# Kernel optimization log

Measured on AMD Instinct MI355X. Metric: run time of the kernel, lower is better.

## Reference

```python
import jax, jax.numpy as jnp
import numpy as np

D_MODEL = 1024
N_HEADS = 16
DEPTH = D_MODEL // N_HEADS
DFF = 4096
B, S = 2, 2048
EPS = 1e-6


def layer_norm(x, gamma, beta):
    m = jnp.mean(x, axis=-1, keepdims=True)
    v = jnp.mean(jnp.square(x - m), axis=-1, keepdims=True)
    return (x - m) * jax.lax.rsqrt(v + EPS) * gamma + beta


def setup_inputs() -> dict:
    key = jax.random.key(0)
    ks = jax.random.split(key, 16)
    s = 0.02
    x = jax.random.normal(ks[0], (B, S, D_MODEL), dtype=jnp.float32)
    # causal mask: 1.0 where attention is NOT allowed (upper triangle)
    mask = (1.0 - jnp.tril(jnp.ones((S, S), dtype=jnp.float32)))[None, None, :, :]
    return {
        "x": x,
        "mask": mask,
        "wq": jax.random.normal(ks[1], (D_MODEL, D_MODEL), jnp.float32) * s,
        "bq": jnp.zeros((D_MODEL,), jnp.float32),
        "wk": jax.random.normal(ks[2], (D_MODEL, D_MODEL), jnp.float32) * s,
        "bk": jnp.zeros((D_MODEL,), jnp.float32),
        "wv": jax.random.normal(ks[3], (D_MODEL, D_MODEL), jnp.float32) * s,
        "bv": jnp.zeros((D_MODEL,), jnp.float32),
        "wo": jax.random.normal(ks[4], (D_MODEL, D_MODEL), jnp.float32) * s,
        "bo": jnp.zeros((D_MODEL,), jnp.float32),
        "g1": jnp.ones((D_MODEL,), jnp.float32),
        "be1": jnp.zeros((D_MODEL,), jnp.float32),
        "w1": jax.random.normal(ks[5], (D_MODEL, DFF), jnp.float32) * s,
        "b1": jnp.zeros((DFF,), jnp.float32),
        "w2": jax.random.normal(ks[6], (DFF, D_MODEL), jnp.float32) * s,
        "b2": jnp.zeros((D_MODEL,), jnp.float32),
        "g2": jnp.ones((D_MODEL,), jnp.float32),
        "be2": jnp.zeros((D_MODEL,), jnp.float32),
    }


def reference(x, mask, wq, bq, wk, bk, wv, bv, wo, bo, g1, be1, w1, b1, w2, b2, g2, be2):
    b, s = x.shape[0], x.shape[1]

    def heads(t):  # [B,S,D_MODEL] -> [B,H,S,depth]
        return t.reshape(b, s, N_HEADS, DEPTH).transpose(0, 2, 1, 3)

    q = heads(x @ wq + bq)
    k = heads(x @ wk + bk)
    v = heads(x @ wv + bv)

    # [B,H,S,S] scores, materialized as in the original
    logits = jnp.einsum("bhqd,bhkd->bhqk", q, k) / jnp.sqrt(jnp.float32(DEPTH))
    logits = logits + mask * (-1e9)
    attn = jax.nn.softmax(logits, axis=-1)
    ctx = jnp.einsum("bhqk,bhkd->bhqd", attn, v)
    ctx = ctx.transpose(0, 2, 1, 3).reshape(b, s, D_MODEL)
    attn_out = ctx @ wo + bo

    out1 = layer_norm(x + attn_out, g1, be1)
    ffn = jax.nn.relu(out1 @ w1 + b1) @ w2 + b2
    out2 = layer_norm(out1 + ffn, g2, be2)
    return out2  # dropout inactive (training=False)
```

## Files before the change

### kernel.cpp

```cpp
#include <hip/hip_runtime.h>
#include <stdint.h>

typedef unsigned short u16;
typedef unsigned int u32;
typedef __attribute__((ext_vector_type(8))) short short8;
typedef __attribute__((ext_vector_type(4))) float f32x4;

#define NHEADS 16
#define SEQ 2048
#define DM 1024
#define MROWS 4096
#define FF 4096

static_assert(sizeof(short8) == 16, "short8 must be 16B");

__device__ __forceinline__ u16 f2b(float f) {
  u32 u = __float_as_uint(f);
  u += 0x7fffu + ((u >> 16) & 1u);
  return (u16)(u >> 16);
}
__device__ __forceinline__ u32 f2b2(float lo, float hi) {
  u32 a = __float_as_uint(lo); a += 0x7fffu + ((a >> 16) & 1u);
  u32 b = __float_as_uint(hi); b += 0x7fffu + ((b >> 16) & 1u);
  return (a >> 16) | (b & 0xffff0000u);
}
__device__ __forceinline__ float b2f(u16 h) { return __uint_as_float(((u32)h) << 16); }

__device__ __forceinline__ void async_cp16(const u16* g, u16* l) {
  __builtin_amdgcn_global_load_lds((const __attribute__((address_space(1))) void*)g,
                                   (__attribute__((address_space(3))) void*)l, 16, 0, 0);
}

__global__ __launch_bounds__(256) void prep_k(const float* __restrict__ x,
                                              const float* __restrict__ wq,
                                              const float* __restrict__ wk,
                                              const float* __restrict__ wv,
                                              const float* __restrict__ wo,
                                              const float* __restrict__ w1,
                                              const float* __restrict__ w2,
                                              u16* __restrict__ xb, u16* __restrict__ btq,
                                              u16* __restrict__ wot, u16* __restrict__ w1t,
                                              u16* __restrict__ w2t) {
  const int bid = blockIdx.x, tid = threadIdx.x;
  if (bid < 4096) {
    const int i = bid * 256 + tid;
    const float4 v = ((const float4*)x)[i];
    uint2 o; o.x = f2b2(v.x, v.y); o.y = f2b2(v.z, v.w);
    ((uint2*)xb)[i] = o;
    return;
  }
  __shared__ float tile[32][33];
  const int tb = bid - 4096;
  const float* in; u16* out; int N, K, n0, k0;
  if (tb < 4096) {
    const int m = tb >> 10, t = tb & 1023;
    if (m == 0) { in = wq; out = btq; }
    else if (m == 1) { in = wk; out = btq + 1024 * 1024; }
    else if (m == 2) { in = wv; out = btq + 2 * 1024 * 1024; }
    else { in = wo; out = wot; }
    N = 1024; K = 1024; n0 = (t & 31) * 32; k0 = (t >> 5) * 32;
  } else if (tb < 8192) {
    const int t = tb - 4096;
    in = w1; out = w1t; N = 4096; K = 1024; n0 = (t & 127) * 32; k0 = (t >> 7) * 32;
  } else {
    const int t = tb - 8192;
    in = w2; out = w2t; N = 1024; K = 4096; n0 = (t & 31) * 32; k0 = (t >> 5) * 32;
  }
  const int tx = tid & 31, ty = tid >> 5;
#pragma unroll
  for (int i = 0; i < 4; i++) {
    const int r = ty + i * 8;
    tile[r][tx] = in[(long)(k0 + r) * N + n0 + tx];
  }
  __syncthreads();
#pragma unroll
  for (int i = 0; i < 4; i++) {
    const int r = ty + i * 8;
    out[(long)(n0 + r) * K + k0 + tx] = f2b(tile[tx][r]);
  }
}

template <typename TIN>
__global__ __launch_bounds__(256) void transpose_bf16(const TIN* __restrict__ in,
                                                      u16* __restrict__ out, const int K,
                                                      const int N, const long isz, const long osz) {
  __shared__ float tile[32][33];
  const TIN* inz = in + (long)blockIdx.z * isz;
  u16* outz = out + (long)blockIdx.z * osz;
  const int n0 = blockIdx.x * 32, k0 = blockIdx.y * 32;
  const int tx = threadIdx.x & 31, ty = threadIdx.x >> 5;
#pragma unroll
  for (int i = 0; i < 4; i++) {
    const int r = ty + i * 8;
    float val;
    if constexpr (sizeof(TIN) == 4) { val = inz[(long)(k0 + r) * N + n0 + tx]; }
    else { val = b2f(inz[(long)(k0 + r) * N + n0 + tx]); }
    tile[r][tx] = val;
  }
  __syncthreads();
#pragma unroll
  for (int i = 0; i < 4; i++) {
    const int r = ty + i * 8;
    outz[(long)(n0 + r) * K + k0 + tx] = f2b(tile[tx][r]);
  }
}

#define BM 128
#define BN 128
#define BK 64
#define EPI_QKV 0
#define EPI_RELUB 2
#define EPI_PART 3

template <int EPI>
__global__ __launch_bounds__(256, 2) void gemm_bt(
    const u16* __restrict__ A, const u16* __restrict__ Bt, const int M, const int N,
    const int KITER, const int LDA, const int KOFF,
    const float* __restrict__ bias0, const float* __restrict__ bias1,
    const float* __restrict__ bias2,
    float* __restrict__ outF, u16* __restrict__ outB, u16* __restrict__ outQ,
    u16* __restrict__ outK, u16* __restrict__ outV) {
  __shared__ u16 As[BM * BK];
  __shared__ u16 Bs[BN * BK];
  const int tid = threadIdx.x;
  const int lane = tid & 63;
  const int wv = tid >> 6;
  const int quad = lane >> 4;
  const int lm = lane & 15;
  const int tn = blockIdx.x * BN;
  const int tm = blockIdx.y * BM;
  const int wr = (wv >> 1) * 64;
  const int wc = (wv & 1) * 64;
  const int wslotbase = tid & ~63;
  const long zoff = (long)blockIdx.z * KOFF;
  const u16* Ap = A + zoff;
  const u16* Btp = Bt + zoff;

  const f32x4 z4 = {0.f, 0.f, 0.f, 0.f};
  f32x4 acc[4][4];
#pragma unroll
  for (int i = 0; i < 4; i++)
#pragma unroll
    for (int j = 0; j < 4; j++) acc[i][j] = z4;

  for (int kk = 0; kk < KITER; kk += BK) {
    __syncthreads();
#pragma unroll
    for (int t = 0; t < 4; t++) {
      const int slot = t * 256 + tid;
      const int row = slot >> 3;
      const int c = (slot & 7) ^ (row & 7);
      async_cp16(Ap + (long)(tm + row) * LDA + kk + c * 8,
                 As + (long)(t * 256 + wslotbase) * 8);
    }
#pragma unroll
    for (int t = 0; t < 4; t++) {
      const int slot = t * 256 + tid;
      const int row = slot >> 3;
      const int c = (slot & 7) ^ (row & 7);
      async_cp16(Btp + (long)(tn + row) * LDA + kk + c * 8,
                 Bs + (long)(t * 256 + wslotbase) * 8);
    }
    __syncthreads();
#pragma unroll
    for (int ks = 0; ks < 2; ks++) {
      short8 af[4], bf[4];
#pragma unroll
      for (int mi = 0; mi < 4; mi++) {
        const int row = wr + mi * 16 + lm;
        const int cc = (4 * ks + quad) ^ (row & 7);
        af[mi] = *(const short8*)(As + row * 64 + cc * 8);
      }
#pragma unroll
      for (int ni = 0; ni < 4; ni++) {
        const int row = wc + ni * 16 + lm;
        const int cc = (4 * ks + quad) ^ (row & 7);
        bf[ni] = *(const short8*)(Bs + row * 64 + cc * 8);
      }
#pragma unroll
      for (int mi = 0; mi < 4; mi++)
#pragma unroll
        for (int ni = 0; ni < 4; ni++)
          acc[mi][ni] =
              __builtin_amdgcn_mfma_f32_16x16x32_bf16(af[mi], bf[ni], acc[mi][ni], 0, 0, 0);
    }
  }

  if constexpr (EPI == EPI_QKV) {
    const int which = tn >> 10;
    const float* bs = which == 0 ? bias0 : (which == 1 ? bias1 : bias2);
    u16* os = which == 0 ? outQ : (which == 1 ? outK : outV);
    const float scale = which == 0 ? 0.125f * 1.44269504f : 1.0f;
#pragma unroll
    for (int ni = 0; ni < 4; ni++) {
      const int n = tn + wc + ni * 16 + lm;
      const int hd = n & 1023;
      const int h = hd >> 6, dep = hd & 63;
      const float bval = bs[hd];
#pragma unroll
      for (int mi = 0; mi < 4; mi++) {
#pragma unroll
        for (int r = 0; r < 4; r++) {
          const int m = tm + wr + mi * 16 + quad * 4 + r;
          const int bb = m >> 11, ss = m & 2047;
          os[(((long)(bb * NHEADS + h) * SEQ + ss) << 6) + dep] =
              f2b((acc[mi][ni][r] + bval) * scale);
        }
      }
    }
  } else if constexpr (EPI == EPI_PART) {
    float* po = outF + (long)blockIdx.z * M * N;
#pragma unroll
    for (int mi = 0; mi < 4; mi++) {
#pragma unroll
      for (int r = 0; r < 4; r++) {
        const int m = tm + wr + mi * 16 + quad * 4 + r;
        const long rowo = (long)m * N;
#pragma unroll
        for (int ni = 0; ni < 4; ni++) {
          const int n = tn + wc + ni * 16 + lm;
          po[rowo + n] = acc[mi][ni][r];
        }
      }
    }
  } else {
#pragma unroll
    for (int mi = 0; mi < 4; mi++) {
#pragma unroll
      for (int r = 0; r < 4; r++) {
        const int m = tm + wr + mi * 16 + quad * 4 + r;
        const long rowo = (long)m * N;
#pragma unroll
        for (int ni = 0; ni < 4; ni++) {
          const int n = tn + wc + ni * 16 + lm;
          const float v = acc[mi][ni][r] + bias0[n];
          outB[rowo + n] = f2b(fmaxf(v, 0.f));
        }
      }
    }
  }
}

__global__ __launch_bounds__(256, 3) void attn_fused(const u16* __restrict__ Q,
                                                     const u16* __restrict__ K,
                                                     const u16* __restrict__ Vt,
                                                     u16* __restrict__ O,
                                                     float* __restrict__ part,
                                                     float* __restrict__ lpart) {
  __shared__ u16 Ks[2][64 * 64];
  __shared__ u16 Vs[2][64 * 64];
  __shared__ u16 Ps[4][16 * 72];
  const int tid = threadIdx.x;
  const int lane = tid & 63, w = tid >> 6, quad = lane >> 4, lm = lane & 15;
  const int bid = blockIdx.x;
  const int idx = bid >> 5, hb = bid & 31;
  const int h = hb & 15, b = hb >> 4;
  int qt, c0, nkl, half;
  if (idx < 32) {
    qt = 16 + (idx >> 1);
    const int nk = qt + 1;
    const int h0 = (nk + 1) >> 1;
    half = idx & 1;
    if (half == 0) { c0 = 0; nkl = h0; } else { c0 = h0; nkl = nk - h0; }
  } else {
    qt = 47 - idx; c0 = 0; nkl = qt + 1; half = -1;
  }
  const long bh = (long)(b * NHEADS + h);
  const u16* Qb = Q + bh * SEQ * 64;
  const u16* Kb = K + bh * SEQ * 64;
  const u16* Vb = Vt + bh * (long)64 * SEQ;
  const int rbase = qt * 64 + w * 16;
  const int wslot = tid & ~63;

  short8 qf[2];
#pragma unroll
  for (int ks = 0; ks < 2; ks++)
    qf[ks] = *(const short8*)(Qb + (long)(rbase + lm) * 64 + ks * 32 + quad * 8);

  const f32x4 z4 = {0.f, 0.f, 0.f, 0.f};
  f32x4 ctx[4];
#pragma unroll
  for (int d = 0; d < 4; d++) ctx[d] = z4;
  float lacc = 0.f;
  u16* myP = (u16*)Ps[w];

  {
    const int k0p = c0 * 64;
#pragma unroll
    for (int i = 0; i < 2; i++) {
      const int slot = i * 256 + tid;
      const int row = slot >> 3;
      const int cg = (slot & 7) ^ (row & 7);
      async_cp16(Kb + (long)(k0p + row) * 64 + cg * 8, Ks[0] + (i * 256 + wslot) * 8);
      async_cp16(Vb + (long)row * SEQ + k0p + cg * 8, Vs[0] + (i * 256 + wslot) * 8);
    }
  }

  for (int t = 0; t < nkl; t++) {
    const int cur = t & 1;
    const int k0 = (c0 + t) * 64;
    __syncthreads();
    if (t + 1 < nkl) {
      const int kn = k0 + 64;
#pragma unroll
      for (int i = 0; i < 2; i++) {
        const int slot = i * 256 + tid;
        const int row = slot >> 3;
        const int cg = (slot & 7) ^ (row & 7);
        async_cp16(Kb + (long)(kn + row) * 64 + cg * 8, Ks[1 - cur] + (i * 256 + wslot) * 8);
        async_cp16(Vb + (long)row * SEQ + kn + cg * 8, Vs[1 - cur] + (i * 256 + wslot) * 8);
      }
    }
    const u16* Kc = Ks[cur];
    const u16* Vc = Vs[cur];
    short8 kf[4][2];
#pragma unroll
    for (int ni = 0; ni < 4; ni++) {
      const int row = ni * 16 + lm;
      const int r8 = row & 7;
#pragma unroll
      for (int ks = 0; ks < 2; ks++) {
        const int cc = (ks * 4 + quad) ^ r8;
        kf[ni][ks] = *(const short8*)(Kc + row * 64 + cc * 8);
      }
    }
    f32x4 sa[4];
#pragma unroll
    for (int i = 0; i < 4; i++) sa[i] = z4;
#pragma unroll
    for (int ks = 0; ks < 2; ks++)
#pragma unroll
      for (int ni = 0; ni < 4; ni++)
        sa[ni] = __builtin_amdgcn_mfma_f32_16x16x32_bf16(kf[ni][ks], qf[ks], sa[ni], 0, 0, 0);
    const int qrow = rbase + lm;
    if (k0 + 63 > rbase) {
#pragma unroll
      for (int ni = 0; ni < 4; ni++)
#pragma unroll
        for (int r = 0; r < 4; r++)
          if (k0 + ni * 16 + quad * 4 + r > qrow) sa[ni][r] = -1e9f;
    }
    float tsum = 0.f;
#pragma unroll
    for (int ni = 0; ni < 4; ni++) {
      const float p0 = exp2f(sa[ni][0]);
      const float p1 = exp2f(sa[ni][1]);
      const float p2 = exp2f(sa[ni][2]);
      const float p3 = exp2f(sa[ni][3]);
      tsum += (p0 + p1) + (p2 + p3);
      uint2 o; o.x = f2b2(p0, p1); o.y = f2b2(p2, p3);
      *(uint2*)(myP + lm * 72 + ni * 16 + quad * 4) = o;
    }
    lacc += tsum;
#pragma unroll
    for (int kc = 0; kc < 2; kc++) {
      const short8 bp = *(const short8*)(myP + lm * 72 + kc * 32 + quad * 8);
#pragma unroll
      for (int dni = 0; dni < 4; dni++) {
        const int row = dni * 16 + lm;
        const int cc = (kc * 4 + quad) ^ (row & 7);
        const short8 vfr = *(const short8*)(Vc + row * 64 + cc * 8);
        ctx[dni] = __builtin_amdgcn_mfma_f32_16x16x32_bf16(vfr, bp, ctx[dni], 0, 0, 0);
      }
    }
  }
  float l = lacc;
  l += __shfl_xor(l, 16);
  l += __shfl_xor(l, 32);
  if (half < 0) {
    const float inv = 1.0f / l;
    const int s = rbase + lm;
    const long base = (long)(b * SEQ + s) * DM + h * 64;
#pragma unroll
    for (int dni = 0; dni < 4; dni++) {
      uint2 o;
      o.x = f2b2(ctx[dni][0] * inv, ctx[dni][1] * inv);
      o.y = f2b2(ctx[dni][2] * inv, ctx[dni][3] * inv);
      *(uint2*)(O + base + dni * 16 + quad * 4) = o;
    }
  } else {
    const long pt = ((long)(hb * 16 + (qt - 16))) * 2 + half;
    float* po = part + pt * 4096 + (w * 16 + lm) * 64;
#pragma unroll
    for (int dni = 0; dni < 4; dni++)
      *(float4*)(po + dni * 16 + quad * 4) =
          make_float4(ctx[dni][0], ctx[dni][1], ctx[dni][2], ctx[dni][3]);
    if (quad == 0) lpart[pt * 64 + w * 16 + lm] = l;
  }
}

__global__ __launch_bounds__(256) void attn_combine(const float* __restrict__ part,
                                                    const float* __restrict__ lpart,
                                                    u16* __restrict__ O) {
  const int g = blockIdx.x;
  const int hb = g >> 4, qtr = g & 15;
  const int h = hb & 15, b = hb >> 4;
  const int qt = 16 + qtr;
  const long pt0 = ((long)(hb * 16 + qtr)) * 2;
  const float* p0 = part + pt0 * 4096;
  const float* p1 = p0 + 4096;
  const float* lp = lpart + pt0 * 64;
  const int tid = threadIdx.x;
  const int row = tid >> 2, d0 = (tid & 3) * 16;
  const float inv = 1.0f / (lp[row] + lp[64 + row]);
  const long off = (long)(b * SEQ + qt * 64 + row) * DM + h * 64 + d0;
  u32 o[8];
#pragma unroll
  for (int i = 0; i < 4; i++) {
    const float4 a = *(const float4*)(p0 + row * 64 + d0 + i * 4);
    const float4 c = *(const float4*)(p1 + row * 64 + d0 + i * 4);
    o[i * 2 + 0] = f2b2((a.x + c.x) * inv, (a.y + c.y) * inv);
    o[i * 2 + 1] = f2b2((a.z + c.z) * inv, (a.w + c.w) * inv);
  }
  *(uint4*)(O + off) = make_uint4(o[0], o[1], o[2], o[3]);
  *(uint4*)(O + off + 8) = make_uint4(o[4], o[5], o[6], o[7]);
}

template <bool WB>
__global__ __launch_bounds__(256) void layernorm2_k(const float* __restrict__ p0,
                                                    const float* __restrict__ p1,
                                                    const float* __restrict__ resid,
                                                    const float* __restrict__ bias,
                                                    const float* __restrict__ gam,
                                                    const float* __restrict__ bet,
                                                    float* __restrict__ outF,
                                                    u16* __restrict__ outB) {
  __shared__ float red[8];
  const int row = blockIdx.x, tid = threadIdx.x;
  const long off = (long)row * DM;
  const float4 a4 = ((const float4*)(p0 + off))[tid];
  const float4 b4v = ((const float4*)(p1 + off))[tid];
  const float4 r4 = ((const float4*)(resid + off))[tid];
  const float4 bi4 = ((const float4*)bias)[tid];
  float4 v;
  v.x = a4.x + b4v.x + r4.x + bi4.x;
  v.y = a4.y + b4v.y + r4.y + bi4.y;
  v.z = a4.z + b4v.z + r4.z + bi4.z;
  v.w = a4.w + b4v.w + r4.w + bi4.w;
  float s1 = v.x + v.y + v.z + v.w;
  float s2 = v.x * v.x + v.y * v.y + v.z * v.z + v.w * v.w;
  s1 += __shfl_xor(s1, 1); s2 += __shfl_xor(s2, 1);
  s1 += __shfl_xor(s1, 2); s2 += __shfl_xor(s2, 2);
  s1 += __shfl_xor(s1, 4); s2 += __shfl_xor(s2, 4);
  s1 += __shfl_xor(s1, 8); s2 += __shfl_xor(s2, 8);
  s1 += __shfl_xor(s1, 16); s2 += __shfl_xor(s2, 16);
  s1 += __shfl_xor(s1, 32); s2 += __shfl_xor(s2, 32);
  if ((tid & 63) == 0) { red[tid >> 6] = s1; red[4 + (tid >> 6)] = s2; }
  __syncthreads();
  const float mean = (red[0] + red[1] + red[2] + red[3]) * (1.f / DM);
  const float ex2 = (red[4] + red[5] + red[6] + red[7]) * (1.f / DM);
  const float var = fmaxf(ex2 - mean * mean, 0.f);
  const float rs = rsqrtf(var + 1e-6f);
  const float4 g4 = ((const float4*)gam)[tid];
  const float4 be4 = ((const float4*)bet)[tid];
  const float o0 = (v.x - mean) * rs * g4.x + be4.x;
  const float o1 = (v.y - mean) * rs * g4.y + be4.y;
  const float o2 = (v.z - mean) * rs * g4.z + be4.z;
  const float o3 = (v.w - mean) * rs * g4.w + be4.w;
  ((float4*)(outF + off))[tid] = make_float4(o0, o1, o2, o3);
  if constexpr (WB) {
    uint2 o; o.x = f2b2(o0, o1); o.y = f2b2(o2, o3);
    ((uint2*)(outB + off))[tid] = o;
  }
}

extern "C" void kernel_launch(void* const* d_in, const int* in_sizes, int n_in,
                              void* d_out, int out_size, void* d_ws, size_t ws_size,
                              hipStream_t stream) {
  (void)in_sizes; (void)n_in; (void)out_size; (void)ws_size;
  const float* x = (const float*)d_in[0];
  const float* wq = (const float*)d_in[2];
  const float* bq = (const float*)d_in[3];
  const float* wk = (const float*)d_in[4];
  const float* bk = (const float*)d_in[5];
  const float* wv = (const float*)d_in[6];
  const float* bv = (const float*)d_in[7];
  const float* wo = (const float*)d_in[8];
  const float* bo = (const float*)d_in[9];
  const float* g1 = (const float*)d_in[10];
  const float* be1 = (const float*)d_in[11];
  const float* w1 = (const float*)d_in[12];
  const float* b1 = (const float*)d_in[13];
  const float* w2 = (const float*)d_in[14];
  const float* b2 = (const float*)d_in[15];
  const float* g2 = (const float*)d_in[16];
  const float* be2 = (const float*)d_in[17];
  float* out = (float*)d_out;
  uint8_t* ws = (uint8_t*)d_ws;
  const size_t MB = 1024ull * 1024ull;
  u16* wot = (u16*)(ws + 0 * MB);
  u16* w1t = (u16*)(ws + 2 * MB);
  u16* w2t = (u16*)(ws + 10 * MB);
  u16* btq = (u16*)(ws + 18 * MB);
  u16* xb  = (u16*)(ws + 24 * MB);
  u16* qb  = (u16*)(ws + 32 * MB);
  u16* kb  = (u16*)(ws + 40 * MB);
  u16* vb  = (u16*)(ws + 48 * MB);
  u16* vt  = (u16*)(ws + 56 * MB);
  u16* ctxb = (u16*)(ws + 64 * MB);
  float* part = (float*)(ws + 72 * MB);
  float* apart = (float*)(ws + 72 * MB);
  float* lpart = (float*)(ws + 89 * MB);
  u16* o1b = (u16*)(ws + 104 * MB);
  float* o1f = (float*)(ws + 112 * MB);
  u16* h1 = (u16*)(ws + 18 * MB);

  prep_k<<<dim3(16384), dim3(256), 0, stream>>>(x, wq, wk, wv, wo, w1, w2, xb, btq, wot,
                                                w1t, w2t);

  gemm_bt<EPI_QKV><<<dim3(24, 32), dim3(256), 0, stream>>>(
      xb, btq, MROWS, 3072, 1024, 1024, 0, bq, bk, bv, nullptr, nullptr, qb, kb, vb);

  transpose_bf16<u16><<<dim3(2, 64, 32), dim3(256), 0, stream>>>(
      vb, vt, 2048, 64, (long)2048 * 64, (long)64 * 2048);

  attn_fused<<<dim3(1536), dim3(256), 0, stream>>>(qb, kb, vt, ctxb, apart, lpart);
  attn_combine<<<dim3(512), dim3(256), 0, stream>>>(apart, lpart, ctxb);

  gemm_bt<EPI_PART><<<dim3(8, 32, 2), dim3(256), 0, stream>>>(
      ctxb, wot, MROWS, 1024, 512, 1024, 512, nullptr, nullptr, nullptr, part, nullptr,
      nullptr, nullptr, nullptr);

  layernorm2_k<true><<<dim3(4096), dim3(256), 0, stream>>>(
      part, part + (long)MROWS * DM, x, bo, g1, be1, o1f, o1b);

  gemm_bt<EPI_RELUB><<<dim3(32, 32), dim3(256), 0, stream>>>(
      o1b, w1t, MROWS, 4096, 1024, 1024, 0, b1, nullptr, nullptr, nullptr, h1, nullptr,
      nullptr, nullptr);

  gemm_bt<EPI_PART><<<dim3(8, 32, 2), dim3(256), 0, stream>>>(
      h1, w2t, MROWS, 1024, 2048, 4096, 2048, nullptr, nullptr, nullptr, part, nullptr,
      nullptr, nullptr, nullptr);

  layernorm2_k<false><<<dim3(4096), dim3(256), 0, stream>>>(
      part, part + (long)MROWS * DM, o1f, b2, g2, be2, out, nullptr);
}
```

Before: 357.7 us.

## Fuse V transpose into QKV epilogue, drop split-K partials, add residual in GEMM

```diff
diff --git a/kernel.cpp b/kernel.cpp
--- a/kernel.cpp
+++ b/kernel.cpp
@@ -23,6 +23,9 @@
   u32 a = __float_as_uint(lo); a += 0x7fffu + ((a >> 16) & 1u);
   u32 b = __float_as_uint(hi); b += 0x7fffu + ((b >> 16) & 1u);
   return (a >> 16) | (b & 0xffff0000u);
+}
+__device__ __forceinline__ u32 f2b2t(float lo, float hi) {
+  return __builtin_amdgcn_perm(__float_as_uint(hi), __float_as_uint(lo), 0x07060302u);
 }
 __device__ __forceinline__ float b2f(u16 h) { return __uint_as_float(((u32)h) << 16); }
 
@@ -80,44 +83,18 @@
   }
 }
 
-template <typename TIN>
-__global__ __launch_bounds__(256) void transpose_bf16(const TIN* __restrict__ in,
-                                                      u16* __restrict__ out, const int K,
-                                                      const int N, const long isz, const long osz) {
-  __shared__ float tile[32][33];
-  const TIN* inz = in + (long)blockIdx.z * isz;
-  u16* outz = out + (long)blockIdx.z * osz;
-  const int n0 = blockIdx.x * 32, k0 = blockIdx.y * 32;
-  const int tx = threadIdx.x & 31, ty = threadIdx.x >> 5;
-#pragma unroll
-  for (int i = 0; i < 4; i++) {
-    const int r = ty + i * 8;
-    float val;
-    if constexpr (sizeof(TIN) == 4) { val = inz[(long)(k0 + r) * N + n0 + tx]; }
-    else { val = b2f(inz[(long)(k0 + r) * N + n0 + tx]); }
-    tile[r][tx] = val;
-  }
-  __syncthreads();
-#pragma unroll
-  for (int i = 0; i < 4; i++) {
-    const int r = ty + i * 8;
-    outz[(long)(n0 + r) * K + k0 + tx] = f2b(tile[tx][r]);
-  }
-}
-
 #define BM 128
 #define BN 128
 #define BK 64
 #define EPI_QKV 0
+#define EPI_ADDRES 1
 #define EPI_RELUB 2
-#define EPI_PART 3
 
 template <int EPI>
 __global__ __launch_bounds__(256, 2) void gemm_bt(
     const u16* __restrict__ A, const u16* __restrict__ Bt, const int M, const int N,
-    const int KITER, const int LDA, const int KOFF,
-    const float* __restrict__ bias0, const float* __restrict__ bias1,
-    const float* __restrict__ bias2,
+    const int K, const float* __restrict__ bias0, const float* __restrict__ bias1,
+    const float* __restrict__ bias2, const float* __restrict__ resid,
     float* __restrict__ outF, u16* __restrict__ outB, u16* __restrict__ outQ,
     u16* __restrict__ outK, u16* __restrict__ outV) {
   __shared__ u16 As[BM * BK];
@@ -132,9 +109,6 @@
   const int wr = (wv >> 1) * 64;
   const int wc = (wv & 1) * 64;
   const int wslotbase = tid & ~63;
-  const long zoff = (long)blockIdx.z * KOFF;
-  const u16* Ap = A + zoff;
-  const u16* Btp = Bt + zoff;
 
   const f32x4 z4 = {0.f, 0.f, 0.f, 0.f};
   f32x4 acc[4][4];
@@ -143,14 +117,14 @@
 #pragma unroll
     for (int j = 0; j < 4; j++) acc[i][j] = z4;
 
-  for (int kk = 0; kk < KITER; kk += BK) {
+  for (int kk = 0; kk < K; kk += BK) {
     __syncthreads();
 #pragma unroll
     for (int t = 0; t < 4; t++) {
       const int slot = t * 256 + tid;
       const int row = slot >> 3;
       const int c = (slot & 7) ^ (row & 7);
-      async_cp16(Ap + (long)(tm + row) * LDA + kk + c * 8,
+      async_cp16(A + (long)(tm + row) * K + kk + c * 8,
                  As + (long)(t * 256 + wslotbase) * 8);
     }
 #pragma unroll
@@ -158,7 +132,7 @@
       const int slot = t * 256 + tid;
       const int row = slot >> 3;
       const int c = (slot & 7) ^ (row & 7);
-      async_cp16(Btp + (long)(tn + row) * LDA + kk + c * 8,
+      async_cp16(Bt + (long)(tn + row) * K + kk + c * 8,
                  Bs + (long)(t * 256 + wslotbase) * 8);
     }
     __syncthreads();
@@ -188,28 +162,46 @@
 
   if constexpr (EPI == EPI_QKV) {
     const int which = tn >> 10;
-    const float* bs = which == 0 ? bias0 : (which == 1 ? bias1 : bias2);
-    u16* os = which == 0 ? outQ : (which == 1 ? outK : outV);
-    const float scale = which == 0 ? 0.125f * 1.44269504f : 1.0f;
-#pragma unroll
-    for (int ni = 0; ni < 4; ni++) {
-      const int n = tn + wc + ni * 16 + lm;
-      const int hd = n & 1023;
-      const int h = hd >> 6, dep = hd & 63;
-      const float bval = bs[hd];
-#pragma unroll
-      for (int mi = 0; mi < 4; mi++) {
-#pragma unroll
-        for (int r = 0; r < 4; r++) {
-          const int m = tm + wr + mi * 16 + quad * 4 + r;
-          const int bb = m >> 11, ss = m & 2047;
-          os[(((long)(bb * NHEADS + h) * SEQ + ss) << 6) + dep] =
-              f2b((acc[mi][ni][r] + bval) * scale);
+    const int bb = tm >> 11;
+    if (which < 2) {
+      const float* bs = which == 0 ? bias0 : bias1;
+      u16* os = which == 0 ? outQ : outK;
+      const float scale = which == 0 ? 0.125f * 1.44269504f : 1.0f;
+#pragma unroll
+      for (int ni = 0; ni < 4; ni++) {
+        const int n = tn + wc + ni * 16 + lm;
+        const int hd = n & 1023;
+        const int h = hd >> 6, dep = hd & 63;
+        const float bval = bs[hd];
+#pragma unroll
+        for (int mi = 0; mi < 4; mi++) {
+#pragma unroll
+          for (int r = 0; r < 4; r++) {
+            const int ss = (tm & 2047) + wr + mi * 16 + quad * 4 + r;
+            os[(((long)(bb * NHEADS + h) * SEQ + ss) << 6) + dep] =
+                f2b((acc[mi][ni][r] + bval) * scale);
+          }
         }
       }
-    }
-  } else if constexpr (EPI == EPI_PART) {
-    float* po = outF + (long)blockIdx.z * M * N;
+    } else {
+#pragma unroll
+      for (int ni = 0; ni < 4; ni++) {
+        const int n = tn + wc + ni * 16 + lm;
+        const int hd = n & 1023;
+        const int h = hd >> 6, dep = hd & 63;
+        const float bval = bias2[hd];
+        u16* vrow = outV + ((long)(bb * NHEADS + h) * 64 + dep) * SEQ;
+#pragma unroll
+        for (int mi = 0; mi < 4; mi++) {
+          const int ss = (tm & 2047) + wr + mi * 16 + quad * 4;
+          uint2 o;
+          o.x = f2b2(acc[mi][ni][0] + bval, acc[mi][ni][1] + bval);
+          o.y = f2b2(acc[mi][ni][2] + bval, acc[mi][ni][3] + bval);
+          *(uint2*)(vrow + ss) = o;
+        }
+      }
+    }
+  } else {
 #pragma unroll
     for (int mi = 0; mi < 4; mi++) {
 #pragma unroll
@@ -219,22 +211,12 @@
 #pragma unroll
         for (int ni = 0; ni < 4; ni++) {
           const int n = tn + wc + ni * 16 + lm;
-          po[rowo + n] = acc[mi][ni][r];
-        }
-      }
-    }
-  } else {
-#pragma unroll
-    for (int mi = 0; mi < 4; mi++) {
-#pragma unroll
-      for (int r = 0; r < 4; r++) {
-        const int m = tm + wr + mi * 16 + quad * 4 + r;
-        const long rowo = (long)m * N;
-#pragma unroll
-        for (int ni = 0; ni < 4; ni++) {
-          const int n = tn + wc + ni * 16 + lm;
           const float v = acc[mi][ni][r] + bias0[n];
-          outB[rowo + n] = f2b(fmaxf(v, 0.f));
+          if constexpr (EPI == EPI_ADDRES) {
+            outF[rowo + n] = v + resid[rowo + n];
+          } else {
+            outB[rowo + n] = f2b(fmaxf(v, 0.f));
+          }
         }
       }
     }
@@ -272,6 +254,18 @@
   const int rbase = qt * 64 + w * 16;
   const int wslot = tid & ~63;
 
+  long kgo[2], vgo[2];
+  int ldso[2];
+#pragma unroll
+  for (int i = 0; i < 2; i++) {
+    const int slot = i * 256 + tid;
+    const int row = slot >> 3;
+    const int cg = (slot & 7) ^ (row & 7);
+    kgo[i] = (long)row * 64 + cg * 8;
+    vgo[i] = (long)row * SEQ + cg * 8;
+    ldso[i] = (i * 256 + wslot) * 8;
+  }
+
   short8 qf[2];
 #pragma unroll
   for (int ks = 0; ks < 2; ks++)
@@ -285,14 +279,11 @@
   u16* myP = (u16*)Ps[w];
 
   {
-    const int k0p = c0 * 64;
+    const long ko = (long)c0 * 64 * 64;
 #pragma unroll
     for (int i = 0; i < 2; i++) {
-      const int slot = i * 256 + tid;
-      const int row = slot >> 3;
-      const int cg = (slot & 7) ^ (row & 7);
-      async_cp16(Kb + (long)(k0p + row) * 64 + cg * 8, Ks[0] + (i * 256 + wslot) * 8);
-      async_cp16(Vb + (long)row * SEQ + k0p + cg * 8, Vs[0] + (i * 256 + wslot) * 8);
+      async_cp16(Kb + ko + kgo[i], Ks[0] + ldso[i]);
+      async_cp16(Vb + c0 * 64 + vgo[i], Vs[0] + ldso[i]);
     }
   }
 
@@ -301,14 +292,11 @@
     const int k0 = (c0 + t) * 64;
     __syncthreads();
     if (t + 1 < nkl) {
-      const int kn = k0 + 64;
+      const long ko = (long)(k0 + 64) * 64;
 #pragma unroll
       for (int i = 0; i < 2; i++) {
-        const int slot = i * 256 + tid;
-        const int row = slot >> 3;
-        const int cg = (slot & 7) ^ (row & 7);
-        async_cp16(Kb + (long)(kn + row) * 64 + cg * 8, Ks[1 - cur] + (i * 256 + wslot) * 8);
-        async_cp16(Vb + (long)row * SEQ + kn + cg * 8, Vs[1 - cur] + (i * 256 + wslot) * 8);
+        async_cp16(Kb + ko + kgo[i], Ks[1 - cur] + ldso[i]);
+        async_cp16(Vb + (k0 + 64) + vgo[i], Vs[1 - cur] + ldso[i]);
       }
     }
     const u16* Kc = Ks[cur];
@@ -348,7 +336,7 @@
       const float p2 = exp2f(sa[ni][2]);
       const float p3 = exp2f(sa[ni][3]);
       tsum += (p0 + p1) + (p2 + p3);
-      uint2 o; o.x = f2b2(p0, p1); o.y = f2b2(p2, p3);
+      uint2 o; o.x = f2b2t(p0, p1); o.y = f2b2t(p2, p3);
       *(uint2*)(myP + lm * 72 + ni * 16 + quad * 4) = o;
     }
     lacc += tsum;
@@ -417,26 +405,15 @@
 }
 
 template <bool WB>
-__global__ __launch_bounds__(256) void layernorm2_k(const float* __restrict__ p0,
-                                                    const float* __restrict__ p1,
-                                                    const float* __restrict__ resid,
-                                                    const float* __restrict__ bias,
-                                                    const float* __restrict__ gam,
-                                                    const float* __restrict__ bet,
-                                                    float* __restrict__ outF,
-                                                    u16* __restrict__ outB) {
+__global__ __launch_bounds__(256) void ln_k(const float* __restrict__ in,
+                                            const float* __restrict__ gam,
+                                            const float* __restrict__ bet,
+                                            float* __restrict__ outF,
+                                            u16* __restrict__ outB) {
   __shared__ float red[8];
   const int row = blockIdx.x, tid = threadIdx.x;
   const long off = (long)row * DM;
-  const float4 a4 = ((const float4*)(p0 + off))[tid];
-  const float4 b4v = ((const float4*)(p1 + off))[tid];
-  const float4 r4 = ((const float4*)(resid + off))[tid];
-  const float4 bi4 = ((const float4*)bias)[tid];
-  float4 v;
-  v.x = a4.x + b4v.x + r4.x + bi4.x;
-  v.y = a4.y + b4v.y + r4.y + bi4.y;
-  v.z = a4.z + b4v.z + r4.z + bi4.z;
-  v.w = a4.w + b4v.w + r4.w + bi4.w;
+  const float4 v = ((const float4*)(in + off))[tid];
   float s1 = v.x + v.y + v.z + v.w;
   float s2 = v.x * v.x + v.y * v.y + v.z * v.z + v.w * v.w;
   s1 += __shfl_xor(s1, 1); s2 += __shfl_xor(s2, 1);
@@ -495,43 +472,38 @@
   u16* xb  = (u16*)(ws + 24 * MB);
   u16* qb  = (u16*)(ws + 32 * MB);
   u16* kb  = (u16*)(ws + 40 * MB);
-  u16* vb  = (u16*)(ws + 48 * MB);
-  u16* vt  = (u16*)(ws + 56 * MB);
-  u16* ctxb = (u16*)(ws + 64 * MB);
-  float* part = (float*)(ws + 72 * MB);
-  float* apart = (float*)(ws + 72 * MB);
-  float* lpart = (float*)(ws + 89 * MB);
+  u16* vt  = (u16*)(ws + 48 * MB);
+  u16* ctxb = (u16*)(ws + 56 * MB);
+  float* apart = (float*)(ws + 64 * MB);
+  float* lpart = (float*)(ws + 81 * MB);
+  float* res1 = (float*)(ws + 88 * MB);
   u16* o1b = (u16*)(ws + 104 * MB);
   float* o1f = (float*)(ws + 112 * MB);
   u16* h1 = (u16*)(ws + 18 * MB);
+  float* res2 = (float*)(ws + 88 * MB);
 
   prep_k<<<dim3(16384), dim3(256), 0, stream>>>(x, wq, wk, wv, wo, w1, w2, xb, btq, wot,
                                                 w1t, w2t);
 
   gemm_bt<EPI_QKV><<<dim3(24, 32), dim3(256), 0, stream>>>(
-      xb, btq, MROWS, 3072, 1024, 1024, 0, bq, bk, bv, nullptr, nullptr, qb, kb, vb);
-
-  transpose_bf16<u16><<<dim3(2, 64, 32), dim3(256), 0, stream>>>(
-      vb, vt, 2048, 64, (long)2048 * 64, (long)64 * 2048);
+      xb, btq, MROWS, 3072, 1024, bq, bk, bv, nullptr, nullptr, nullptr, qb, kb, vt);
 
   attn_fused<<<dim3(1536), dim3(256), 0, stream>>>(qb, kb, vt, ctxb, apart, lpart);
   attn_combine<<<dim3(512), dim3(256), 0, stream>>>(apart, lpart, ctxb);
 
-  gemm_bt<EPI_PART><<<dim3(8, 32, 2), dim3(256), 0, stream>>>(
-      ctxb, wot, MROWS, 1024, 512, 1024, 512, nullptr, nullptr, nullptr, part, nullptr,
-      nullptr, nullptr, nullptr);
-
-  layernorm2_k<true><<<dim3(4096), dim3(256), 0, stream>>>(
-      part, part + (long)MROWS * DM, x, bo, g1, be1, o1f, o1b);
+  gemm_bt<EPI_ADDRES><<<dim3(8, 32), dim3(256), 0, stream>>>(
+      ctxb, wot, MROWS, 1024, 1024, bo, nullptr, nullptr, x, res1, nullptr, nullptr,
+      nullptr, nullptr);
+
+  ln_k<true><<<dim3(4096), dim3(256), 0, stream>>>(res1, g1, be1, o1f, o1b);
 
   gemm_bt<EPI_RELUB><<<dim3(32, 32), dim3(256), 0, stream>>>(
-      o1b, w1t, MROWS, 4096, 1024, 1024, 0, b1, nullptr, nullptr, nullptr, h1, nullptr,
+      o1b, w1t, MROWS, 4096, 1024, b1, nullptr, nullptr, nullptr, nullptr, h1, nullptr,
       nullptr, nullptr);
 
-  gemm_bt<EPI_PART><<<dim3(8, 32, 2), dim3(256), 0, stream>>>(
-      h1, w2t, MROWS, 1024, 2048, 4096, 2048, nullptr, nullptr, nullptr, part, nullptr,
-      nullptr, nullptr, nullptr);
-
-  layernorm2_k<false><<<dim3(4096), dim3(256), 0, stream>>>(
-      part, part + (long)MROWS * DM, o1f, b2, g2, be2, out, nullptr);
-}
+  gemm_bt<EPI_ADDRES><<<dim3(8, 32), dim3(256), 0, stream>>>(
+      h1, w2t, MROWS, 1024, 4096, b2, nullptr, nullptr, o1f, res2, nullptr, nullptr,
+      nullptr, nullptr);
+
+  ln_k<false><<<dim3(4096), dim3(256), 0, stream>>>(res2, g2, be2, out, nullptr);
+}
```

New measurement: 359.8 us. About the same (+0.6%).
